# Kernel tuning notes

Hardware: AMD Instinct MI355X
Metric: run time of the kernel (lower is better)

Reference implementation:

```python
import jax, jax.numpy as jnp
import numpy as np

FIELD_DIMS = [100000, 1000, 100, 50]
NUM_FEATURES = 12
NUM_CAT = len(FIELD_DIMS)
NUM_CONT = NUM_FEATURES - NUM_CAT
D = 32            # embed_dim
HID = [64, 32]
B, T = 1024, 200
BN_EPS = 1e-5


def setup_inputs() -> dict:
    key = jax.random.key(0)
    ks = jax.random.split(key, 32)
    # x: [B, T, F]; first NUM_CAT cols are integer category ids stored as float
    cat_cols = [jax.random.randint(ks[i], (B, T, 1), 0, FIELD_DIMS[i]).astype(jnp.float32)
                for i in range(NUM_CAT)]
    cont_cols = jax.random.normal(ks[4], (B, T, NUM_CONT), dtype=jnp.float32)
    x = jnp.concatenate(cat_cols + [cont_cols], axis=-1)
    s = 0.05
    inp = {"x": x}
    for i, fd in enumerate(FIELD_DIMS):
        inp[f"emb{i}"] = jax.random.normal(ks[5 + i], (fd, D), dtype=jnp.float32) * s
        inp[f"lin{i}"] = jax.random.normal(ks[9 + i], (fd, D), dtype=jnp.float32) * s
    # Conv1d(1, D, 1) per continuous field == per-field affine map scalar -> D
    inp["cont_w"]  = jax.random.normal(ks[13], (NUM_CONT, D), dtype=jnp.float32) * s
    inp["cont_b"]  = jax.random.normal(ks[14], (NUM_CONT, D), dtype=jnp.float32) * s
    inp["clin_w"]  = jax.random.normal(ks[15], (NUM_CONT, D), dtype=jnp.float32) * s
    inp["clin_b"]  = jax.random.normal(ks[16], (NUM_CONT, D), dtype=jnp.float32) * s
    inp["fin_bias"] = jnp.zeros((D,), dtype=jnp.float32)
    # DNN tower: kernel_size-1 Conv1d == dense over channel dim
    dims = [NUM_FEATURES * D] + HID
    for li in range(len(HID)):
        fan_in = dims[li]
        inp[f"w{li+1}"] = jax.random.normal(ks[17 + 4 * li], (HID[li], fan_in), dtype=jnp.float32) / np.sqrt(fan_in)
        inp[f"b{li+1}"] = jnp.zeros((HID[li],), dtype=jnp.float32)
        inp[f"g{li+1}"] = jnp.ones((HID[li],), dtype=jnp.float32)
        inp[f"beta{li+1}"] = jnp.zeros((HID[li],), dtype=jnp.float32)
    inp["w_out"] = jax.random.normal(ks[30], (D, HID[-1]), dtype=jnp.float32) / np.sqrt(HID[-1])
    inp["b_out"] = jnp.zeros((D,), dtype=jnp.float32)
    return inp


def _batchnorm(h, g, b):
    # training-mode BN over (batch, time), biased variance (torch default)
    mu = h.mean(axis=(0, 1))
    var = h.var(axis=(0, 1))
    return g * (h - mu) * jax.lax.rsqrt(var + BN_EPS) + b


def reference(x, emb0, emb1, emb2, emb3, lin0, lin1, lin2, lin3,
              cont_w, cont_b, clin_w, clin_b, fin_bias,
              w1, b1, g1, beta1, w2, b2, g2, beta2, w_out, b_out):
    embs = [emb0, emb1, emb2, emb3]
    lins = [lin0, lin1, lin2, lin3]
    cat_idx = x[..., :NUM_CAT].astype(jnp.int32)          # [B,T,C]
    xc = x[..., NUM_CAT:]                                  # [B,T,Nc]

    # per-field embeddings -> [B,T,F,D]
    cat_emb = jnp.stack([embs[i][cat_idx[..., i]] for i in range(NUM_CAT)], axis=2)
    cont_emb = xc[..., None] * cont_w + cont_b             # [B,T,Nc,D]
    emb_all = jnp.concatenate([cat_emb, cont_emb], axis=2)  # [B,T,F,D]

    # FM pairwise interaction (sum-of-squares trick)
    s = emb_all.sum(axis=2)                                # [B,T,D]
    interaction = 0.5 * (s * s - (emb_all * emb_all).sum(axis=2))

    # linear terms
    lin_cat = sum(lins[i][cat_idx[..., i]] for i in range(NUM_CAT))      # [B,T,D]
    lin_cont = (xc[..., None] * clin_w + clin_b).sum(axis=2)             # [B,T,D]
    linear = lin_cat + lin_cont + fin_bias

    # DNN tower (k=1 convs == dense over F*D channels); dropout omitted (eval)
    h = emb_all.reshape(B, T, NUM_FEATURES * D)
    h = jax.nn.relu(_batchnorm(h @ w1.T + b1, g1, beta1))
    h = jax.nn.relu(_batchnorm(h @ w2.T + b2, g2, beta2))
    dnn = h @ w_out.T + b_out                              # [B,T,D]

    return linear + interaction + dnn                      # [B,T,D]
```

## Files before the change

### kernel.cpp

```cpp
#include <hip/hip_runtime.h>
#include <hip/hip_bf16.h>

typedef __hip_bfloat16 bf16;

#define ROWS 204800
#define N_INV (1.0f / 204800.0f)

__device__ float g_stats[256];
__device__ float g_E1_0[100000 * 64];
__device__ float g_E1_1[1000 * 64];
__device__ float g_E1_2[100 * 64];
__device__ float g_E1_3[50 * 64];
__device__ float g_U[8 * 64];
__device__ float g_Vb[64];
__device__ float g_bn1[128];
__device__ float g_bn2[64];
__device__ bf16  g_h1p[ROWS * 64];
__device__ bf16  g_h2p[ROWS * 32];

__device__ __forceinline__ int clampi(int v, int hi) {
    return v < 0 ? 0 : (v > hi ? hi : v);
}
__device__ __forceinline__ float rl_f(float v, int l) {
    return __uint_as_float((unsigned int)__builtin_amdgcn_readlane((int)__float_as_uint(v), l));
}

__global__ __launch_bounds__(64) void precompute_kernel(
    const float* __restrict__ emb1, const float* __restrict__ emb2, const float* __restrict__ emb3,
    const float* __restrict__ cont_w, const float* __restrict__ cont_b,
    const float* __restrict__ w1, const float* __restrict__ b1)
{
    int b = blockIdx.x;
    int k = threadIdx.x;
    __shared__ float row[32];

    if (b < 1150) {
        const float* tab; float* out; int i, colOff;
        if (b < 1000)      { tab = emb1; out = g_E1_1; i = b;        colOff = 32; }
        else if (b < 1100) { tab = emb2; out = g_E1_2; i = b - 1000; colOff = 64; }
        else               { tab = emb3; out = g_E1_3; i = b - 1100; colOff = 96; }
        if (k < 32) row[k] = tab[i * 32 + k];
        __syncthreads();
        const float* wr = w1 + k * 384 + colOff;
        float acc = 0.f;
        #pragma unroll
        for (int d = 0; d < 32; ++d) acc = fmaf(row[d], wr[d], acc);
        out[i * 64 + k] = acc;
    } else {
        g_stats[k]       = 0.f;
        g_stats[k + 64]  = 0.f;
        g_stats[k + 128] = 0.f;
        g_stats[k + 192] = 0.f;

        float vb = b1[k];
        #pragma unroll
        for (int j = 0; j < 8; ++j) {
            const float* wr = w1 + k * 384 + (4 + j) * 32;
            float u = 0.f;
            #pragma unroll
            for (int d = 0; d < 32; ++d) {
                float w = wr[d];
                u  = fmaf(cont_w[j * 32 + d], w, u);
                vb = fmaf(cont_b[j * 32 + d], w, vb);
            }
            g_U[j * 64 + k] = u;
        }
        g_Vb[k] = vb;
    }
}

__global__ __launch_bounds__(256) void e10_kernel(
    const float* __restrict__ emb0, const float* __restrict__ w1)
{
    int lane = threadIdx.x & 63;
    int wv   = threadIdx.x >> 6;

    float w1col[32];
    {
        const float4* wr = (const float4*)(w1 + lane * 384);
        #pragma unroll
        for (int q = 0; q < 8; ++q) {
            float4 v = wr[q];
            w1col[4*q+0] = v.x; w1col[4*q+1] = v.y;
            w1col[4*q+2] = v.z; w1col[4*q+3] = v.w;
        }
    }

    for (int i = blockIdx.x * 4 + wv; i < 100000; i += gridDim.x * 4) {
        float e = emb0[i * 32 + (lane & 31)];
        float a0 = 0.f, a1 = 0.f, a2 = 0.f, a3 = 0.f;
        #pragma unroll
        for (int dd = 0; dd < 32; dd += 4) {
            a0 = fmaf(rl_f(e, dd + 0), w1col[dd + 0], a0);
            a1 = fmaf(rl_f(e, dd + 1), w1col[dd + 1], a1);
            a2 = fmaf(rl_f(e, dd + 2), w1col[dd + 2], a2);
            a3 = fmaf(rl_f(e, dd + 3), w1col[dd + 3], a3);
        }
        g_E1_0[i * 64 + lane] = (a0 + a1) + (a2 + a3);
    }
}

__global__ __launch_bounds__(256) void phase1_kernel(
    const float* __restrict__ x,
    const float* __restrict__ emb0, const float* __restrict__ lin0,
    const float* __restrict__ emb1, const float* __restrict__ lin1,
    const float* __restrict__ emb2, const float* __restrict__ lin2,
    const float* __restrict__ emb3, const float* __restrict__ lin3,
    const float* __restrict__ cont_w, const float* __restrict__ cont_b,
    const float* __restrict__ clin_w, const float* __restrict__ clin_b,
    const float* __restrict__ fin_bias,
    float* __restrict__ fm_out)
{
    __shared__ float lsum[64], lsq[64];

    int tid  = threadIdx.x;
    int lane = tid & 63;
    int wv   = tid >> 6;
    int d    = lane & 31;
    bool lo  = lane < 32;

    if (tid < 64) { lsum[tid] = 0.f; lsq[tid] = 0.f; }
    __syncthreads();

    float uk[8];
    #pragma unroll
    for (int j = 0; j < 8; ++j) uk[j] = g_U[j * 64 + lane];
    float vbk = g_Vb[lane];

    float p1[8], p2[8], fb = 0.f;
    if (lo) {
        #pragma unroll
        for (int j = 0; j < 8; ++j) { p1[j] = cont_w[j * 32 + d]; p2[j] = cont_b[j * 32 + d]; }
    } else {
        #pragma unroll
        for (int j = 0; j < 8; ++j) { p1[j] = clin_w[j * 32 + d]; p2[j] = clin_b[j * 32 + d]; }
        fb = fin_bias[d];
    }

    const float* T0 = lo ? emb0 : lin0;
    const float* T1 = lo ? emb1 : lin1;
    const float* T2 = lo ? emb2 : lin2;
    const float* T3 = lo ? emb3 : lin3;

    int gw   = blockIdx.x * 4 + wv;
    int base = gw * 16;

    float xs[4];
    #pragma unroll
    for (int g = 0; g < 4; ++g)
        xs[g] = (lane < 48) ? x[(base + 4 * g) * 12 + lane] : 0.f;

    float ss = 0.f, qq = 0.f;

    #pragma unroll
    for (int g = 0; g < 4; ++g) {
        int rb = base + 4 * g;

        int i0[4], i1[4], i2[4], i3[4];
        #pragma unroll
        for (int t = 0; t < 4; ++t) {
            int f = t * 12;
            i0[t] = clampi((int)rl_f(xs[g], f + 0), 99999);
            i1[t] = clampi((int)rl_f(xs[g], f + 1), 999);
            i2[t] = clampi((int)rl_f(xs[g], f + 2), 99);
            i3[t] = clampi((int)rl_f(xs[g], f + 3), 49);
        }

        float ga[4], gb[4], gc[4], gd[4], E0[4], t1[4], t2[4], t3[4];
        #pragma unroll
        for (int t = 0; t < 4; ++t) {
            ga[t] = T0[i0[t] * 32 + d];
            gb[t] = T1[i1[t] * 32 + d];
            gc[t] = T2[i2[t] * 32 + d];
            gd[t] = T3[i3[t] * 32 + d];
            E0[t] = g_E1_0[i0[t] * 64 + lane];
            t1[t] = g_E1_1[i1[t] * 64 + lane];
            t2[t] = g_E1_2[i2[t] * 64 + lane];
            t3[t] = g_E1_3[i3[t] * 64 + lane];
        }

        #pragma unroll
        for (int t = 0; t < 4; ++t) {
            int r = rb + t;
            int fo = t * 12 + 4;
            float xc[8];
            #pragma unroll
            for (int j = 0; j < 8; ++j) xc[j] = rl_f(xs[g], fo + j);

            float half_val;
            if (lo) {
                float s0 = ga[t] + gb[t], s1 = gc[t] + gd[t];
                float q0 = fmaf(ga[t], ga[t], gb[t] * gb[t]);
                float q1 = fmaf(gc[t], gc[t], gd[t] * gd[t]);
                #pragma unroll
                for (int j = 0; j < 8; ++j) {
                    float ce = fmaf(xc[j], p1[j], p2[j]);
                    if (j & 1) { s1 += ce; q1 = fmaf(ce, ce, q1); }
                    else       { s0 += ce; q0 = fmaf(ce, ce, q0); }
                }
                float s = s0 + s1;
                half_val = 0.5f * (s * s - (q0 + q1));
            } else {
                float l0 = ga[t] + gb[t] + fb, l1 = gc[t] + gd[t];
                #pragma unroll
                for (int j = 0; j < 8; ++j) {
                    if (j & 1) l1 = fmaf(xc[j], p1[j], l1 + p2[j]);
                    else       l0 = fmaf(xc[j], p1[j], l0 + p2[j]);
                }
                half_val = l0 + l1;
            }
            float other = __shfl(half_val, lane | 32);
            if (lo) fm_out[r * 32 + d] = half_val + other;

            float h1 = ((vbk + E0[t]) + (t1[t] + t2[t])) + t3[t];
            #pragma unroll
            for (int j = 0; j < 8; ++j) h1 = fmaf(xc[j], uk[j], h1);

            g_h1p[r * 64 + lane] = __float2bfloat16(h1);
            ss += h1;
            qq = fmaf(h1, h1, qq);
        }
    }

    atomicAdd(&lsum[lane], ss);
    atomicAdd(&lsq[lane], qq);
    __syncthreads();
    if (tid < 64) {
        atomicAdd(&g_stats[tid], lsum[tid]);
        atomicAdd(&g_stats[64 + tid], lsq[tid]);
    }
}

__global__ __launch_bounds__(64) void bnprep1_kernel(
    const float* __restrict__ g1, const float* __restrict__ beta1)
{
    int k = threadIdx.x;
    float mu  = g_stats[k] * N_INV;
    float var = g_stats[64 + k] * N_INV - mu * mu;
    float a   = g1[k] * rsqrtf(var + 1e-5f);
    g_bn1[k]      = a;
    g_bn1[64 + k] = beta1[k] - a * mu;
}

__global__ __launch_bounds__(256) void phase2_kernel(
    const float* __restrict__ w2, const float* __restrict__ b2)
{
    int tid  = threadIdx.x;
    int lane = tid & 63;
    int wv   = tid >> 6;
    size_t row = (size_t)(blockIdx.x * 4 + wv) * 64 + lane;

    const uint4* hrow = (const uint4*)(g_h1p + row * 64);

    float acc[32];
    #pragma unroll
    for (int m = 0; m < 32; ++m) acc[m] = 0.f;

    #pragma unroll
    for (int half = 0; half < 2; ++half) {
        uint4 u[4];
        #pragma unroll
        for (int q = 0; q < 4; ++q) u[q] = hrow[half * 4 + q];

        float y[32];
        #pragma unroll
        for (int q = 0; q < 4; ++q) {
            unsigned int w4[4] = {u[q].x, u[q].y, u[q].z, u[q].w};
            #pragma unroll
            for (int j = 0; j < 4; ++j) {
                int i  = q * 4 + j;
                int ch = half * 32 + 2 * i;
                float f0 = __uint_as_float(w4[j] << 16);
                float f1 = __uint_as_float(w4[j] & 0xffff0000u);
                y[2*i]     = fmaxf(0.f, fmaf(g_bn1[ch],     f0, g_bn1[64 + ch]));
                y[2*i + 1] = fmaxf(0.f, fmaf(g_bn1[ch + 1], f1, g_bn1[64 + ch + 1]));
            }
        }

        #pragma unroll
        for (int m = 0; m < 32; ++m) {
            const float* wr = w2 + m * 64 + half * 32;
            float a0 = 0.f, a1 = 0.f, a2 = 0.f, a3 = 0.f;
            #pragma unroll
            for (int k = 0; k < 32; k += 4) {
                a0 = fmaf(y[k + 0], wr[k + 0], a0);
                a1 = fmaf(y[k + 1], wr[k + 1], a1);
                a2 = fmaf(y[k + 2], wr[k + 2], a2);
                a3 = fmaf(y[k + 3], wr[k + 3], a3);
            }
            acc[m] += (a0 + a1) + (a2 + a3);
        }
    }

    uint4 o[4];
    unsigned int* ow = (unsigned int*)o;
    #pragma unroll
    for (int i = 0; i < 16; ++i) {
        unsigned int lo16 = (unsigned int)__bfloat16_as_ushort(__float2bfloat16(acc[2*i]     + b2[2*i]));
        unsigned int hi16 = (unsigned int)__bfloat16_as_ushort(__float2bfloat16(acc[2*i + 1] + b2[2*i + 1]));
        ow[i] = lo16 | (hi16 << 16);
    }
    uint4* orow = (uint4*)(g_h2p + row * 32);
    #pragma unroll
    for (int q = 0; q < 4; ++q) orow[q] = o[q];
}

__global__ __launch_bounds__(256) void red2_kernel()
{
    __shared__ float ls[64];
    int tid = threadIdx.x;
    if (tid < 64) ls[tid] = 0.f;
    __syncthreads();

    const unsigned int* p = (const unsigned int*)g_h2p;
    int cp = tid & 15;
    float s0 = 0.f, q0 = 0.f, s1 = 0.f, q1 = 0.f;
    for (int i = blockIdx.x * 256 + tid; i < ROWS * 16; i += 256 * 256) {
        unsigned int u = p[i];
        float f0 = __uint_as_float(u << 16);
        float f1 = __uint_as_float(u & 0xffff0000u);
        s0 += f0; q0 = fmaf(f0, f0, q0);
        s1 += f1; q1 = fmaf(f1, f1, q1);
    }
    atomicAdd(&ls[2*cp],      s0);
    atomicAdd(&ls[2*cp + 1],  s1);
    atomicAdd(&ls[32 + 2*cp], q0);
    atomicAdd(&ls[33 + 2*cp], q1);
    __syncthreads();
    if (tid < 32)            atomicAdd(&g_stats[128 + tid], ls[tid]);
    else if (tid < 64)       atomicAdd(&g_stats[160 + (tid - 32)], ls[tid]);
}

__global__ __launch_bounds__(32) void bnprep2_kernel(
    const float* __restrict__ g2, const float* __restrict__ beta2)
{
    int m = threadIdx.x;
    float mu  = g_stats[128 + m] * N_INV;
    float var = g_stats[160 + m] * N_INV - mu * mu;
    float a   = g2[m] * rsqrtf(var + 1e-5f);
    g_bn2[m]      = a;
    g_bn2[32 + m] = beta2[m] - a * mu;
}

__global__ __launch_bounds__(256) void phase3_kernel(
    const float* __restrict__ w_out, const float* __restrict__ b_out,
    float* __restrict__ out)
{
    int tid  = threadIdx.x;
    int lane = tid & 63;
    int wv   = tid >> 6;
    size_t row = (size_t)(blockIdx.x * 4 + wv) * 64 + lane;

    const uint4* hrow = (const uint4*)(g_h2p + row * 32);
    uint4 u[4];
    #pragma unroll
    for (int q = 0; q < 4; ++q) u[q] = hrow[q];

    float y2[32];
    #pragma unroll
    for (int q = 0; q < 4; ++q) {
        unsigned int w4[4] = {u[q].x, u[q].y, u[q].z, u[q].w};
        #pragma unroll
        for (int j = 0; j < 4; ++j) {
            int i = q * 4 + j;
            float f0 = __uint_as_float(w4[j] << 16);
            float f1 = __uint_as_float(w4[j] & 0xffff0000u);
            y2[2*i]     = fmaxf(0.f, fmaf(g_bn2[2*i],     f0, g_bn2[32 + 2*i]));
            y2[2*i + 1] = fmaxf(0.f, fmaf(g_bn2[2*i + 1], f1, g_bn2[32 + 2*i + 1]));
        }
    }

    float res[32];
    #pragma unroll
    for (int dd = 0; dd < 32; ++dd) {
        const float* wr = w_out + dd * 32;
        float a0 = b_out[dd], a1 = 0.f, a2 = 0.f, a3 = 0.f;
        #pragma unroll
        for (int k = 0; k < 32; k += 4) {
            a0 = fmaf(y2[k + 0], wr[k + 0], a0);
            a1 = fmaf(y2[k + 1], wr[k + 1], a1);
            a2 = fmaf(y2[k + 2], wr[k + 2], a2);
            a3 = fmaf(y2[k + 3], wr[k + 3], a3);
        }
        res[dd] = (a0 + a1) + (a2 + a3);
    }

    float4* orow = (float4*)(out + row * 32);
    #pragma unroll
    for (int q = 0; q < 8; ++q) {
        float4 f = orow[q];
        orow[q] = make_float4(res[4*q+0] + f.x, res[4*q+1] + f.y,
                              res[4*q+2] + f.z, res[4*q+3] + f.w);
    }
}

extern "C" void kernel_launch(void* const* d_in, const int* in_sizes, int n_in,
                              void* d_out, int out_size, void* d_ws, size_t ws_size,
                              hipStream_t stream) {
    (void)in_sizes; (void)n_in; (void)out_size; (void)d_ws; (void)ws_size;

    const float* x       = (const float*)d_in[0];
    const float* emb0    = (const float*)d_in[1];
    const float* lin0    = (const float*)d_in[2];
    const float* emb1    = (const float*)d_in[3];
    const float* lin1    = (const float*)d_in[4];
    const float* emb2    = (const float*)d_in[5];
    const float* lin2    = (const float*)d_in[6];
    const float* emb3    = (const float*)d_in[7];
    const float* lin3    = (const float*)d_in[8];
    const float* cont_w  = (const float*)d_in[9];
    const float* cont_b  = (const float*)d_in[10];
    const float* clin_w  = (const float*)d_in[11];
    const float* clin_b  = (const float*)d_in[12];
    const float* fin_bias= (const float*)d_in[13];
    const float* w1      = (const float*)d_in[14];
    const float* b1      = (const float*)d_in[15];
    const float* g1      = (const float*)d_in[16];
    const float* beta1   = (const float*)d_in[17];
    const float* w2      = (const float*)d_in[18];
    const float* b2      = (const float*)d_in[19];
    const float* g2      = (const float*)d_in[20];
    const float* beta2   = (const float*)d_in[21];
    const float* w_out   = (const float*)d_in[22];
    const float* b_out   = (const float*)d_in[23];

    float* outp = (float*)d_out;

    hipLaunchKernelGGL(precompute_kernel, dim3(1151), dim3(64), 0, stream,
                       emb1, emb2, emb3, cont_w, cont_b, w1, b1);

    hipLaunchKernelGGL(e10_kernel, dim3(1600), dim3(256), 0, stream, emb0, w1);

    hipLaunchKernelGGL(phase1_kernel, dim3(3200), dim3(256), 0, stream,
                       x, emb0, lin0, emb1, lin1, emb2, lin2, emb3, lin3,
                       cont_w, cont_b, clin_w, clin_b, fin_bias,
                       outp);

    hipLaunchKernelGGL(bnprep1_kernel, dim3(1), dim3(64), 0, stream, g1, beta1);

    hipLaunchKernelGGL(phase2_kernel, dim3(800), dim3(256), 0, stream, w2, b2);

    hipLaunchKernelGGL(red2_kernel, dim3(256), dim3(256), 0, stream);

    hipLaunchKernelGGL(bnprep2_kernel, dim3(1), dim3(32), 0, stream, g2, beta2);

    hipLaunchKernelGGL(phase3_kernel, dim3(800), dim3(256), 0, stream,
                       w_out, b_out, outp);
}
```

Measured before the change: 341.7 us.

## Store emb0 W1 projection in bf16 and issue all phase1 gathers up front

Stores the precomputed emb0·W1 projection table as bf16 instead of fp32. This halves its footprint and the bytes moved by the large random gather. Phase1 now gives each wave 8 rows instead of 16, loads indices for all 8 rows and issues every gather before any compute, doubles the grid, and adds a launch-bounds occupancy hint. This raises memory-level parallelism, at the cost of extra bf16 rounding in the first hidden layer pre-activation and more live registers.

```diff
diff --git a/kernel.cpp b/kernel.cpp
--- a/kernel.cpp
+++ b/kernel.cpp
@@ -7,7 +7,7 @@
 #define N_INV (1.0f / 204800.0f)
 
 __device__ float g_stats[256];
-__device__ float g_E1_0[100000 * 64];
+__device__ bf16  g_E1_0b[100000 * 64];
 __device__ float g_E1_1[1000 * 64];
 __device__ float g_E1_2[100 * 64];
 __device__ float g_E1_3[50 * 64];
@@ -23,6 +23,9 @@
 }
 __device__ __forceinline__ float rl_f(float v, int l) {
     return __uint_as_float((unsigned int)__builtin_amdgcn_readlane((int)__float_as_uint(v), l));
+}
+__device__ __forceinline__ float us2f(unsigned short u) {
+    return __uint_as_float(((unsigned int)u) << 16);
 }
 
 __global__ __launch_bounds__(64) void precompute_kernel(
@@ -96,11 +99,11 @@
             a2 = fmaf(rl_f(e, dd + 2), w1col[dd + 2], a2);
             a3 = fmaf(rl_f(e, dd + 3), w1col[dd + 3], a3);
         }
-        g_E1_0[i * 64 + lane] = (a0 + a1) + (a2 + a3);
-    }
-}
-
-__global__ __launch_bounds__(256) void phase1_kernel(
+        g_E1_0b[i * 64 + lane] = __float2bfloat16((a0 + a1) + (a2 + a3));
+    }
+}
+
+__global__ __launch_bounds__(256, 4) void phase1_kernel(
     const float* __restrict__ x,
     const float* __restrict__ emb0, const float* __restrict__ lin0,
     const float* __restrict__ emb1, const float* __restrict__ lin1,
@@ -143,83 +146,79 @@
     const float* T3 = lo ? emb3 : lin3;
 
     int gw   = blockIdx.x * 4 + wv;
-    int base = gw * 16;
-
-    float xs[4];
-    #pragma unroll
-    for (int g = 0; g < 4; ++g)
-        xs[g] = (lane < 48) ? x[(base + 4 * g) * 12 + lane] : 0.f;
+    int base = gw * 8;
+
+    float xa = (lane < 48) ? x[base * 12 + lane] : 0.f;
+    float xb = (lane < 48) ? x[base * 12 + 48 + lane] : 0.f;
+
+    int i0[8], i1[8], i2[8], i3[8];
+    #pragma unroll
+    for (int it = 0; it < 8; ++it) {
+        float s = (it < 4) ? xa : xb;
+        int   f = (it < 4) ? it * 12 : it * 12 - 48;
+        i0[it] = clampi((int)rl_f(s, f + 0), 99999);
+        i1[it] = clampi((int)rl_f(s, f + 1), 999);
+        i2[it] = clampi((int)rl_f(s, f + 2), 99);
+        i3[it] = clampi((int)rl_f(s, f + 3), 49);
+    }
+
+    float ga[8], gb[8], gc[8], gd[8], t1[8], t2[8], t3[8];
+    unsigned short e0u[8];
+    #pragma unroll
+    for (int it = 0; it < 8; ++it) {
+        ga[it]  = T0[i0[it] * 32 + d];
+        gb[it]  = T1[i1[it] * 32 + d];
+        gc[it]  = T2[i2[it] * 32 + d];
+        gd[it]  = T3[i3[it] * 32 + d];
+        e0u[it] = ((const unsigned short*)g_E1_0b)[i0[it] * 64 + lane];
+        t1[it]  = g_E1_1[i1[it] * 64 + lane];
+        t2[it]  = g_E1_2[i2[it] * 64 + lane];
+        t3[it]  = g_E1_3[i3[it] * 64 + lane];
+    }
 
     float ss = 0.f, qq = 0.f;
 
     #pragma unroll
-    for (int g = 0; g < 4; ++g) {
-        int rb = base + 4 * g;
-
-        int i0[4], i1[4], i2[4], i3[4];
-        #pragma unroll
-        for (int t = 0; t < 4; ++t) {
-            int f = t * 12;
-            i0[t] = clampi((int)rl_f(xs[g], f + 0), 99999);
-            i1[t] = clampi((int)rl_f(xs[g], f + 1), 999);
-            i2[t] = clampi((int)rl_f(xs[g], f + 2), 99);
-            i3[t] = clampi((int)rl_f(xs[g], f + 3), 49);
-        }
-
-        float ga[4], gb[4], gc[4], gd[4], E0[4], t1[4], t2[4], t3[4];
-        #pragma unroll
-        for (int t = 0; t < 4; ++t) {
-            ga[t] = T0[i0[t] * 32 + d];
-            gb[t] = T1[i1[t] * 32 + d];
-            gc[t] = T2[i2[t] * 32 + d];
-            gd[t] = T3[i3[t] * 32 + d];
-            E0[t] = g_E1_0[i0[t] * 64 + lane];
-            t1[t] = g_E1_1[i1[t] * 64 + lane];
-            t2[t] = g_E1_2[i2[t] * 64 + lane];
-            t3[t] = g_E1_3[i3[t] * 64 + lane];
-        }
-
-        #pragma unroll
-        for (int t = 0; t < 4; ++t) {
-            int r = rb + t;
-            int fo = t * 12 + 4;
-            float xc[8];
+    for (int it = 0; it < 8; ++it) {
+        int r  = base + it;
+        float xs = (it < 4) ? xa : xb;
+        int   fo = ((it < 4) ? it * 12 : it * 12 - 48) + 4;
+        float xc[8];
+        #pragma unroll
+        for (int j = 0; j < 8; ++j) xc[j] = rl_f(xs, fo + j);
+
+        float half_val;
+        if (lo) {
+            float s0 = ga[it] + gb[it], s1 = gc[it] + gd[it];
+            float q0 = fmaf(ga[it], ga[it], gb[it] * gb[it]);
+            float q1 = fmaf(gc[it], gc[it], gd[it] * gd[it]);
             #pragma unroll
-            for (int j = 0; j < 8; ++j) xc[j] = rl_f(xs[g], fo + j);
-
-            float half_val;
-            if (lo) {
-                float s0 = ga[t] + gb[t], s1 = gc[t] + gd[t];
-                float q0 = fmaf(ga[t], ga[t], gb[t] * gb[t]);
-                float q1 = fmaf(gc[t], gc[t], gd[t] * gd[t]);
-                #pragma unroll
-                for (int j = 0; j < 8; ++j) {
-                    float ce = fmaf(xc[j], p1[j], p2[j]);
-                    if (j & 1) { s1 += ce; q1 = fmaf(ce, ce, q1); }
-                    else       { s0 += ce; q0 = fmaf(ce, ce, q0); }
-                }
-                float s = s0 + s1;
-                half_val = 0.5f * (s * s - (q0 + q1));
-            } else {
-                float l0 = ga[t] + gb[t] + fb, l1 = gc[t] + gd[t];
-                #pragma unroll
-                for (int j = 0; j < 8; ++j) {
-                    if (j & 1) l1 = fmaf(xc[j], p1[j], l1 + p2[j]);
-                    else       l0 = fmaf(xc[j], p1[j], l0 + p2[j]);
-                }
-                half_val = l0 + l1;
+            for (int j = 0; j < 8; ++j) {
+                float ce = fmaf(xc[j], p1[j], p2[j]);
+                if (j & 1) { s1 += ce; q1 = fmaf(ce, ce, q1); }
+                else       { s0 += ce; q0 = fmaf(ce, ce, q0); }
             }
-            float other = __shfl(half_val, lane | 32);
-            if (lo) fm_out[r * 32 + d] = half_val + other;
-
-            float h1 = ((vbk + E0[t]) + (t1[t] + t2[t])) + t3[t];
+            float s = s0 + s1;
+            half_val = 0.5f * (s * s - (q0 + q1));
+        } else {
+            float l0 = ga[it] + gb[it] + fb, l1 = gc[it] + gd[it];
             #pragma unroll
-            for (int j = 0; j < 8; ++j) h1 = fmaf(xc[j], uk[j], h1);
-
-            g_h1p[r * 64 + lane] = __float2bfloat16(h1);
-            ss += h1;
-            qq = fmaf(h1, h1, qq);
-        }
+            for (int j = 0; j < 8; ++j) {
+                if (j & 1) l1 = fmaf(xc[j], p1[j], l1 + p2[j]);
+                else       l0 = fmaf(xc[j], p1[j], l0 + p2[j]);
+            }
+            half_val = l0 + l1;
+        }
+        float other = __shfl(half_val, lane | 32);
+        if (lo) fm_out[r * 32 + d] = half_val + other;
+
+        float h1 = ((vbk + us2f(e0u[it])) + (t1[it] + t2[it])) + t3[it];
+        #pragma unroll
+        for (int j = 0; j < 8; ++j) h1 = fmaf(xc[j], uk[j], h1);
+
+        g_h1p[r * 64 + lane] = __float2bfloat16(h1);
+        ss += h1;
+        qq = fmaf(h1, h1, qq);
     }
 
     atomicAdd(&lsum[lane], ss);
@@ -431,7 +430,7 @@
 
     hipLaunchKernelGGL(e10_kernel, dim3(1600), dim3(256), 0, stream, emb0, w1);
 
-    hipLaunchKernelGGL(phase1_kernel, dim3(3200), dim3(256), 0, stream,
+    hipLaunchKernelGGL(phase1_kernel, dim3(6400), dim3(256), 0, stream,
                        x, emb0, lin0, emb1, lin1, emb2, lin2, emb3, lin3,
                        cont_w, cont_b, clin_w, clin_b, fin_bias,
                        outp);
```

Result: slower. 440.5 us (+28.9%).

## Store E1_0 in bf16, prefetch gathers one group ahead, fold BN prep into consumers

Applied to the files above, without the earlier changes.

The precomputed first-layer projection of the large emb0 table is now stored as bf16 instead of fp32, halving its footprint and the bytes each gather reads. Phase1 now issues the next group's gathers before computing the current group, using double-buffered registers to hide gather latency. The two single-block BN-prep kernels are removed and their scale/shift math is recomputed per block into shared memory inside phase2 and phase3, saving two launches. The cost is bf16 rounding of the E1_0 term, higher register pressure, and redundant per-block BN prep work.

```diff
diff --git a/kernel.cpp b/kernel.cpp
--- a/kernel.cpp
+++ b/kernel.cpp
@@ -7,14 +7,12 @@
 #define N_INV (1.0f / 204800.0f)
 
 __device__ float g_stats[256];
-__device__ float g_E1_0[100000 * 64];
+__device__ bf16  g_E1_0b[100000 * 64];
 __device__ float g_E1_1[1000 * 64];
 __device__ float g_E1_2[100 * 64];
 __device__ float g_E1_3[50 * 64];
 __device__ float g_U[8 * 64];
 __device__ float g_Vb[64];
-__device__ float g_bn1[128];
-__device__ float g_bn2[64];
 __device__ bf16  g_h1p[ROWS * 64];
 __device__ bf16  g_h2p[ROWS * 32];
 
@@ -23,6 +21,9 @@
 }
 __device__ __forceinline__ float rl_f(float v, int l) {
     return __uint_as_float((unsigned int)__builtin_amdgcn_readlane((int)__float_as_uint(v), l));
+}
+__device__ __forceinline__ float us2f(unsigned short u) {
+    return __uint_as_float(((unsigned int)u) << 16);
 }
 
 __global__ __launch_bounds__(64) void precompute_kernel(
@@ -96,7 +97,7 @@
             a2 = fmaf(rl_f(e, dd + 2), w1col[dd + 2], a2);
             a3 = fmaf(rl_f(e, dd + 3), w1col[dd + 3], a3);
         }
-        g_E1_0[i * 64 + lane] = (a0 + a1) + (a2 + a3);
+        g_E1_0b[i * 64 + lane] = __float2bfloat16((a0 + a1) + (a2 + a3));
     }
 }
 
@@ -150,58 +151,62 @@
     for (int g = 0; g < 4; ++g)
         xs[g] = (lane < 48) ? x[(base + 4 * g) * 12 + lane] : 0.f;
 
+    float ga[2][4], gb[2][4], gc[2][4], gd[2][4], t1[2][4], t2[2][4], t3[2][4];
+    unsigned short e0u[2][4];
+
+    auto issue = [&](int g, int s) {
+        #pragma unroll
+        for (int t = 0; t < 4; ++t) {
+            int f  = t * 12;
+            int i0 = clampi((int)rl_f(xs[g], f + 0), 99999);
+            int i1 = clampi((int)rl_f(xs[g], f + 1), 999);
+            int i2 = clampi((int)rl_f(xs[g], f + 2), 99);
+            int i3 = clampi((int)rl_f(xs[g], f + 3), 49);
+            ga[s][t]  = T0[i0 * 32 + d];
+            gb[s][t]  = T1[i1 * 32 + d];
+            gc[s][t]  = T2[i2 * 32 + d];
+            gd[s][t]  = T3[i3 * 32 + d];
+            e0u[s][t] = ((const unsigned short*)g_E1_0b)[i0 * 64 + lane];
+            t1[s][t]  = g_E1_1[i1 * 64 + lane];
+            t2[s][t]  = g_E1_2[i2 * 64 + lane];
+            t3[s][t]  = g_E1_3[i3 * 64 + lane];
+        }
+    };
+
+    issue(0, 0);
+
     float ss = 0.f, qq = 0.f;
 
     #pragma unroll
     for (int g = 0; g < 4; ++g) {
-        int rb = base + 4 * g;
-
-        int i0[4], i1[4], i2[4], i3[4];
+        int s = g & 1;
+        if (g < 3) issue(g + 1, (g + 1) & 1);
+
         #pragma unroll
         for (int t = 0; t < 4; ++t) {
-            int f = t * 12;
-            i0[t] = clampi((int)rl_f(xs[g], f + 0), 99999);
-            i1[t] = clampi((int)rl_f(xs[g], f + 1), 999);
-            i2[t] = clampi((int)rl_f(xs[g], f + 2), 99);
-            i3[t] = clampi((int)rl_f(xs[g], f + 3), 49);
-        }
-
-        float ga[4], gb[4], gc[4], gd[4], E0[4], t1[4], t2[4], t3[4];
-        #pragma unroll
-        for (int t = 0; t < 4; ++t) {
-            ga[t] = T0[i0[t] * 32 + d];
-            gb[t] = T1[i1[t] * 32 + d];
-            gc[t] = T2[i2[t] * 32 + d];
-            gd[t] = T3[i3[t] * 32 + d];
-            E0[t] = g_E1_0[i0[t] * 64 + lane];
-            t1[t] = g_E1_1[i1[t] * 64 + lane];
-            t2[t] = g_E1_2[i2[t] * 64 + lane];
-            t3[t] = g_E1_3[i3[t] * 64 + lane];
-        }
-
-        #pragma unroll
-        for (int t = 0; t < 4; ++t) {
-            int r = rb + t;
+            int r  = base + 4 * g + t;
             int fo = t * 12 + 4;
             float xc[8];
             #pragma unroll
             for (int j = 0; j < 8; ++j) xc[j] = rl_f(xs[g], fo + j);
 
+            float va = ga[s][t], vb = gb[s][t], vc = gc[s][t], vd = gd[s][t];
+
             float half_val;
             if (lo) {
-                float s0 = ga[t] + gb[t], s1 = gc[t] + gd[t];
-                float q0 = fmaf(ga[t], ga[t], gb[t] * gb[t]);
-                float q1 = fmaf(gc[t], gc[t], gd[t] * gd[t]);
+                float s0 = va + vb, s1 = vc + vd;
+                float q0 = fmaf(va, va, vb * vb);
+                float q1 = fmaf(vc, vc, vd * vd);
                 #pragma unroll
                 for (int j = 0; j < 8; ++j) {
                     float ce = fmaf(xc[j], p1[j], p2[j]);
                     if (j & 1) { s1 += ce; q1 = fmaf(ce, ce, q1); }
                     else       { s0 += ce; q0 = fmaf(ce, ce, q0); }
                 }
-                float s = s0 + s1;
-                half_val = 0.5f * (s * s - (q0 + q1));
+                float sfull = s0 + s1;
+                half_val = 0.5f * (sfull * sfull - (q0 + q1));
             } else {
-                float l0 = ga[t] + gb[t] + fb, l1 = gc[t] + gd[t];
+                float l0 = va + vb + fb, l1 = vc + vd;
                 #pragma unroll
                 for (int j = 0; j < 8; ++j) {
                     if (j & 1) l1 = fmaf(xc[j], p1[j], l1 + p2[j]);
@@ -212,7 +217,7 @@
             float other = __shfl(half_val, lane | 32);
             if (lo) fm_out[r * 32 + d] = half_val + other;
 
-            float h1 = ((vbk + E0[t]) + (t1[t] + t2[t])) + t3[t];
+            float h1 = ((vbk + us2f(e0u[s][t])) + (t1[s][t] + t2[s][t])) + t3[s][t];
             #pragma unroll
             for (int j = 0; j < 8; ++j) h1 = fmaf(xc[j], uk[j], h1);
 
@@ -231,21 +236,21 @@
     }
 }
 
-__global__ __launch_bounds__(64) void bnprep1_kernel(
+__global__ __launch_bounds__(256) void phase2_kernel(
+    const float* __restrict__ w2, const float* __restrict__ b2,
     const float* __restrict__ g1, const float* __restrict__ beta1)
 {
-    int k = threadIdx.x;
-    float mu  = g_stats[k] * N_INV;
-    float var = g_stats[64 + k] * N_INV - mu * mu;
-    float a   = g1[k] * rsqrtf(var + 1e-5f);
-    g_bn1[k]      = a;
-    g_bn1[64 + k] = beta1[k] - a * mu;
-}
-
-__global__ __launch_bounds__(256) void phase2_kernel(
-    const float* __restrict__ w2, const float* __restrict__ b2)
-{
+    __shared__ float sa[64], sc[64];
     int tid  = threadIdx.x;
+    if (tid < 64) {
+        float mu  = g_stats[tid] * N_INV;
+        float var = g_stats[64 + tid] * N_INV - mu * mu;
+        float a   = g1[tid] * rsqrtf(var + 1e-5f);
+        sa[tid] = a;
+        sc[tid] = beta1[tid] - a * mu;
+    }
+    __syncthreads();
+
     int lane = tid & 63;
     int wv   = tid >> 6;
     size_t row = (size_t)(blockIdx.x * 4 + wv) * 64 + lane;
@@ -272,8 +277,8 @@
                 int ch = half * 32 + 2 * i;
                 float f0 = __uint_as_float(w4[j] << 16);
                 float f1 = __uint_as_float(w4[j] & 0xffff0000u);
-                y[2*i]     = fmaxf(0.f, fmaf(g_bn1[ch],     f0, g_bn1[64 + ch]));
-                y[2*i + 1] = fmaxf(0.f, fmaf(g_bn1[ch + 1], f1, g_bn1[64 + ch + 1]));
+                y[2*i]     = fmaxf(0.f, fmaf(sa[ch],     f0, sc[ch]));
+                y[2*i + 1] = fmaxf(0.f, fmaf(sa[ch + 1], f1, sc[ch + 1]));
             }
         }
 
@@ -331,22 +336,22 @@
     else if (tid < 64)       atomicAdd(&g_stats[160 + (tid - 32)], ls[tid]);
 }
 
-__global__ __launch_bounds__(32) void bnprep2_kernel(
-    const float* __restrict__ g2, const float* __restrict__ beta2)
-{
-    int m = threadIdx.x;
-    float mu  = g_stats[128 + m] * N_INV;
-    float var = g_stats[160 + m] * N_INV - mu * mu;
-    float a   = g2[m] * rsqrtf(var + 1e-5f);
-    g_bn2[m]      = a;
-    g_bn2[32 + m] = beta2[m] - a * mu;
-}
-
 __global__ __launch_bounds__(256) void phase3_kernel(
     const float* __restrict__ w_out, const float* __restrict__ b_out,
+    const float* __restrict__ g2, const float* __restrict__ beta2,
     float* __restrict__ out)
 {
+    __shared__ float sa[32], sc[32];
     int tid  = threadIdx.x;
+    if (tid < 32) {
+        float mu  = g_stats[128 + tid] * N_INV;
+        float var = g_stats[160 + tid] * N_INV - mu * mu;
+        float a   = g2[tid] * rsqrtf(var + 1e-5f);
+        sa[tid] = a;
+        sc[tid] = beta2[tid] - a * mu;
+    }
+    __syncthreads();
+
     int lane = tid & 63;
     int wv   = tid >> 6;
     size_t row = (size_t)(blockIdx.x * 4 + wv) * 64 + lane;
@@ -365,8 +370,8 @@
             int i = q * 4 + j;
             float f0 = __uint_as_float(w4[j] << 16);
             float f1 = __uint_as_float(w4[j] & 0xffff0000u);
-            y2[2*i]     = fmaxf(0.f, fmaf(g_bn2[2*i],     f0, g_bn2[32 + 2*i]));
-            y2[2*i + 1] = fmaxf(0.f, fmaf(g_bn2[2*i + 1], f1, g_bn2[32 + 2*i + 1]));
+            y2[2*i]     = fmaxf(0.f, fmaf(sa[2*i],     f0, sc[2*i]));
+            y2[2*i + 1] = fmaxf(0.f, fmaf(sa[2*i + 1], f1, sc[2*i + 1]));
         }
     }
 
@@ -436,14 +441,11 @@
                        cont_w, cont_b, clin_w, clin_b, fin_bias,
                        outp);
 
-    hipLaunchKernelGGL(bnprep1_kernel, dim3(1), dim3(64), 0, stream, g1, beta1);
-
-    hipLaunchKernelGGL(phase2_kernel, dim3(800), dim3(256), 0, stream, w2, b2);
+    hipLaunchKernelGGL(phase2_kernel, dim3(800), dim3(256), 0, stream,
+                       w2, b2, g1, beta1);
 
     hipLaunchKernelGGL(red2_kernel, dim3(256), dim3(256), 0, stream);
 
-    hipLaunchKernelGGL(bnprep2_kernel, dim3(1), dim3(32), 0, stream, g2, beta2);
-
     hipLaunchKernelGGL(phase3_kernel, dim3(800), dim3(256), 0, stream,
-                       w_out, b_out, outp);
-}
+                       w_out, b_out, g2, beta2, outp);
+}
```

New measurement: 335.9 us. About the same (-1.7%).
